# Optimization experiments

Hardware: AMD Instinct MI355X
Metric: run time of the kernel (lower is better)

The kernel has to match this reference:

```python
import jax, jax.numpy as jnp
import numpy as np

N_NODES = 50000
N_EDGES = 800000
IN_DIM = 256     # state_size
HID = 256        # hidden_dim
ACT = 64         # action_size


def gcn_conv(x, src, dst, norm, W, b):
    # PyG GCNConv: out[dst] += norm_e * (x @ W)[src]; then + bias
    h = x @ W                               # [N, out]
    msg = h[src] * norm[:, None]            # [E+N, out]
    agg = jax.ops.segment_sum(msg, dst, num_segments=N_NODES)
    return agg + b


def gcn_norm(edge_index):
    # add self-loops, symmetric normalization deg^-1/2[src]*deg^-1/2[dst]
    loops = jnp.arange(N_NODES, dtype=edge_index.dtype)
    src = jnp.concatenate([edge_index[0], loops])
    dst = jnp.concatenate([edge_index[1], loops])
    deg = jax.ops.segment_sum(jnp.ones_like(dst, dtype=jnp.float32), dst,
                              num_segments=N_NODES)
    dinv = jnp.where(deg > 0, jax.lax.rsqrt(deg), 0.0)
    norm = dinv[src] * dinv[dst]            # [E+N]
    return src, dst, norm


def setup_inputs() -> dict:
    key = jax.random.key(0)
    ks = jax.random.split(key, 12)
    x = jax.random.normal(ks[0], (N_NODES, IN_DIM), dtype=jnp.float32)
    edge_index = jax.random.randint(ks[1], (2, N_EDGES), 0, N_NODES, dtype=jnp.int64)

    def glorot(k, shape):
        lim = float(np.sqrt(6.0 / (shape[0] + shape[1])))
        return jax.random.uniform(k, shape, jnp.float32, -lim, lim)

    return {
        "x": x, "edge_index": edge_index,
        "W1": glorot(ks[2], (IN_DIM, HID)), "b1": jnp.zeros((HID,), jnp.float32),
        "W2": glorot(ks[3], (HID, HID)),    "b2": jnp.zeros((HID,), jnp.float32),
        "fcW1": glorot(ks[4], (HID, HID)),  "fcb1": jnp.zeros((HID,), jnp.float32),
        "fcW2": glorot(ks[5], (HID, HID)),  "fcb2": jnp.zeros((HID,), jnp.float32),
        "fcW3": glorot(ks[6], (HID, ACT)),  "fcb3": jnp.zeros((ACT,), jnp.float32),
    }


def reference(x, edge_index, W1, b1, W2, b2, fcW1, fcb1, fcW2, fcb2, fcW3, fcb3):
    src, dst, norm = gcn_norm(edge_index)
    h = jax.nn.relu(gcn_conv(x, src, dst, norm, W1, b1))   # GNNLayer 1
    h = jax.nn.relu(gcn_conv(h, src, dst, norm, W2, b2))   # GNNLayer 2
    g = jax.nn.relu(jnp.mean(h, axis=0)[None, :])          # [1, HID]
    g = jax.nn.relu(g @ fcW1 + fcb1)
    g = jax.nn.relu(g @ fcW2 + fcb2)
    return g @ fcW3 + fcb3                                 # [1, ACT]
```

## Files before the change

### kernel.cpp

```cpp
#include <hip/hip_runtime.h>

#define N_NODES 50000
#define N_EDGES 800000
#define DIM 256
#define ACT 64
#define SCAN_B 256
#define SCAN_NB ((N_NODES + SCAN_B - 1) / SCAN_B)
#define SLICE_ELEMS ((size_t)N_NODES * 32)
#define AGG_CHUNKS 512
#define NPC ((N_NODES + AGG_CHUNKS - 1) / AGG_CHUNKS)
#define CSR_MAX (N_EDGES + 16 * N_NODES)

typedef __attribute__((ext_vector_type(8))) short short8_t;
typedef __attribute__((ext_vector_type(4))) float f32x4;
typedef __attribute__((ext_vector_type(4))) unsigned short ushort4_t;

__device__ __forceinline__ unsigned short f2b(float x) {
    unsigned u = __float_as_uint(x);
    unsigned r = u + 0x7FFFu + ((u >> 16) & 1u);
    return (unsigned short)(r >> 16);
}


__global__ __launch_bounds__(256) void k_cvt_x(const float* __restrict__ x,
                                               unsigned short* __restrict__ xb) {
    int i = blockIdx.x * blockDim.x + threadIdx.x;
    const int TOT = N_NODES * DIM / 8;
    if (i >= TOT) return;
    const float4* src = (const float4*)(x) + (size_t)i * 2;
    float4 a = src[0], b = src[1];
    int row = i >> 5;
    int col0 = (i << 3) & 255;
    int slice = col0 >> 5, within = col0 & 31;
    ushort4_t lo, hi;
    lo.x = f2b(a.x); lo.y = f2b(a.y); lo.z = f2b(a.z); lo.w = f2b(a.w);
    hi.x = f2b(b.x); hi.y = f2b(b.y); hi.z = f2b(b.z); hi.w = f2b(b.w);
    ushort4_t* dst = (ushort4_t*)(xb + (size_t)slice * SLICE_ELEMS + (size_t)row * 32 + within);
    dst[0] = lo; dst[1] = hi;
}

__global__ __launch_bounds__(256) void k_cvt_wt2(const float* __restrict__ W1,
                                                 const float* __restrict__ W2,
                                                 unsigned short* __restrict__ W1t,
                                                 unsigned short* __restrict__ W2t) {
    int b = blockIdx.x;
    const float* W = (b < 256) ? W1 : W2;
    unsigned short* Wt = (b < 256) ? W1t : W2t;
    int i = (b & 255) * 256 + threadIdx.x;
    int k = i >> 8, n = i & 255;
    Wt[n * DIM + k] = f2b(W[k * DIM + n]);
}


__global__ void k_deg_count(const int* __restrict__ ei, int* degi) {
    int e = blockIdx.x * blockDim.x + threadIdx.x;
    if (e < N_EDGES) atomicAdd(&degi[ei[N_EDGES + e]], 1);
}


__global__ __launch_bounds__(SCAN_B) void k_scan_local(const int* __restrict__ degi,
                                                       int* lexc, int* btot) {
    __shared__ int sm[SCAN_B];
    int t = threadIdx.x;
    int i = blockIdx.x * SCAN_B + t;
    int v = (i < N_NODES) ? ((degi[i] + 16) & ~15) : 0;
    sm[t] = v;
    __syncthreads();
#pragma unroll
    for (int off = 1; off < SCAN_B; off <<= 1) {
        int u = (t >= off) ? sm[t - off] : 0;
        __syncthreads();
        sm[t] += u;
        __syncthreads();
    }
    if (i < N_NODES) lexc[i] = sm[t] - v;
    if (t == SCAN_B - 1) btot[blockIdx.x] = sm[t];
}

__global__ __launch_bounds__(SCAN_B) void k_scan_tops(const int* __restrict__ btot,
                                                      int* bbase, int* rowstart) {
    __shared__ int sm[SCAN_B];
    int t = threadIdx.x;
    int v = (t < SCAN_NB) ? btot[t] : 0;
    sm[t] = v;
    __syncthreads();
#pragma unroll
    for (int off = 1; off < SCAN_B; off <<= 1) {
        int u = (t >= off) ? sm[t - off] : 0;
        __syncthreads();
        sm[t] += u;
        __syncthreads();
    }
    if (t < SCAN_NB) bbase[t] = sm[t] - v;
    if (t == SCAN_NB - 1) rowstart[N_NODES] = sm[t];
}

__global__ __launch_bounds__(SCAN_B) void k_scan_apply(const int* __restrict__ degi,
                                                       const int* __restrict__ lexc,
                                                       const int* __restrict__ bbase,
                                                       int* rowstart, int* fillpos,
                                                       float* dinv, int2* csr_pair) {
    int i = blockIdx.x * SCAN_B + threadIdx.x;
    if (i >= N_NODES) return;
    int rs = bbase[blockIdx.x] + lexc[i];
    rowstart[i] = rs;
    int d = degi[i] + 1;
    float di = rsqrtf((float)d);
    dinv[i] = di;
    int2 p; p.x = i << 6; p.y = __float_as_int(di * di);
    csr_pair[rs] = p;
    fillpos[i] = rs + 1;
}

__global__ void k_fill_edge(const int* __restrict__ ei,
                            const float* __restrict__ dinv, int* fillpos,
                            int2* csr_pair) {
    int e = blockIdx.x * blockDim.x + threadIdx.x;
    if (e < N_EDGES) {
        int s = ei[e];
        int d = ei[N_EDGES + e];
        int p = atomicAdd(&fillpos[d], 1);
        int2 pr; pr.x = s << 6; pr.y = __float_as_int(dinv[s] * dinv[d]);
        csr_pair[p] = pr;
    }
}


__global__ __launch_bounds__(256) void k_gemm_mfma(const unsigned short* __restrict__ A,
                                                   const unsigned short* __restrict__ Wt,
                                                   unsigned short* __restrict__ H,
                                                   int M) {
    __shared__ char lds[40960];
    char* AsB = lds;
    char* BsB = lds + 8192;

    int tid = threadIdx.x;
    int w = tid >> 6;
    int l = tid & 63;
    int r0 = blockIdx.x * 64;

    f32x4 acc[4][4];
#pragma unroll
    for (int i = 0; i < 4; ++i)
#pragma unroll
        for (int j = 0; j < 4; ++j) acc[i][j] = (f32x4)(0.f);

    for (int kt = 0; kt < 4; ++kt) {
        int k0 = kt * 64;
#pragma unroll
        for (int i = 0; i < 2; ++i) {
            int c = tid + i * 256;
            int row = c >> 3, kc = c & 7;
            int k = k0 + kc * 8;
            int slice = k >> 5, within = k & 31;
            int g = r0 + row; if (g >= M) g = M - 1;
            short8_t v = *(const short8_t*)(A + (size_t)slice * SLICE_ELEMS + (size_t)g * 32 + within);
            int off = (row * 128 + kc * 16) ^ ((row & 7) << 4);
            *(short8_t*)(AsB + off) = v;
        }
#pragma unroll
        for (int i = 0; i < 8; ++i) {
            int c = tid + i * 256;
            int n = c >> 3, kc = c & 7;
            short8_t v = *(const short8_t*)(Wt + n * DIM + k0 + kc * 8);
            int off = (n * 128 + kc * 16) ^ ((n & 7) << 4);
            *(short8_t*)(BsB + off) = v;
        }
        __syncthreads();

#pragma unroll
        for (int kf = 0; kf < 2; ++kf) {
            int kb = kf * 64 + (l >> 4) * 16;
            short8_t a[4], b[4];
#pragma unroll
            for (int fm = 0; fm < 4; ++fm) {
                int ra = fm * 16 + (l & 15);
                a[fm] = *(const short8_t*)(AsB + ((ra * 128 + kb) ^ ((ra & 7) << 4)));
            }
#pragma unroll
            for (int fn = 0; fn < 4; ++fn) {
                int nb = w * 64 + fn * 16 + (l & 15);
                b[fn] = *(const short8_t*)(BsB + ((nb * 128 + kb) ^ ((nb & 7) << 4)));
            }
#pragma unroll
            for (int fm = 0; fm < 4; ++fm)
#pragma unroll
                for (int fn = 0; fn < 4; ++fn)
                    acc[fm][fn] = __builtin_amdgcn_mfma_f32_16x16x32_bf16(
                        a[fm], b[fn], acc[fm][fn], 0, 0, 0);
        }
        __syncthreads();
    }

#pragma unroll
    for (int fm = 0; fm < 4; ++fm) {
#pragma unroll
        for (int i = 0; i < 4; ++i) {
            int row = r0 + fm * 16 + ((l >> 4) << 2) + i;
            if (row >= M) continue;
#pragma unroll
            for (int fn = 0; fn < 4; ++fn) {
                int col = w * 64 + fn * 16 + (l & 15);
                int slice = col >> 5;
                H[(size_t)slice * SLICE_ELEMS + (size_t)row * 32 + (col & 31)] = f2b(acc[fm][fn][i]);
            }
        }
    }
}


__global__ __launch_bounds__(256) void k_agg_sliced(const unsigned short* __restrict__ H,
                                                    const int* __restrict__ rowstart,
                                                    const int2* __restrict__ csr_pair,
                                                    const float* __restrict__ bias,
                                                    unsigned short* __restrict__ X,
                                                    float* __restrict__ gsum,
                                                    int write_out) {
    __shared__ long long pbuf[32][2][17];
    int slice = blockIdx.x & 7;
    int chunk = blockIdx.x >> 3;
    int g = threadIdx.x >> 3;
    int lane = threadIdx.x & 7;
    const char* Hb = (const char*)(H + (size_t)slice * SLICE_ELEMS) + (lane << 3);
    unsigned short* Xs = X + (size_t)slice * SLICE_ELEMS;
    int d0 = slice * 32 + lane * 4;
    float4 bb = *(const float4*)&bias[d0];
    float c0 = 0.f, c1 = 0.f, c2 = 0.f, c3 = 0.f;
    int nEnd = (chunk + 1) * NPC; if (nEnd > N_NODES) nEnd = N_NODES;
    for (int n = chunk * NPC + g; n < nEnd; n += 32) {
        int beg = rowstart[n], end = rowstart[n + 1];
        float a0 = 0.f, a1 = 0.f, a2 = 0.f, a3 = 0.f;
        int4 u = *(const int4*)(csr_pair + beg + lane * 2);
        int r = 0;
        for (int e = beg; e < end; e += 16, ++r) {
            int enext = (e + 16 < end) ? e + 16 : e;
            int4 un = *(const int4*)(csr_pair + enext + lane * 2);
            long long* pb = &pbuf[g][r & 1][0];
            *(int4*)(pb + lane * 2) = u;
#pragma unroll
            for (int i = 0; i < 16; ++i) {
                long long pv = pb[i];
                unsigned off = (unsigned)(int)pv;
                float nm = __int_as_float((int)(pv >> 32));
                uint2 q = *(const uint2*)(Hb + off);
                a0 = fmaf(nm, __uint_as_float(q.x << 16), a0);
                a1 = fmaf(nm, __uint_as_float(q.x & 0xFFFF0000u), a1);
                a2 = fmaf(nm, __uint_as_float(q.y << 16), a2);
                a3 = fmaf(nm, __uint_as_float(q.y & 0xFFFF0000u), a3);
            }
            u = un;
        }
        float o0 = fmaxf(a0 + bb.x, 0.f);
        float o1 = fmaxf(a1 + bb.y, 0.f);
        float o2 = fmaxf(a2 + bb.z, 0.f);
        float o3 = fmaxf(a3 + bb.w, 0.f);
        if (write_out) {
            ushort4_t o; o.x = f2b(o0); o.y = f2b(o1); o.z = f2b(o2); o.w = f2b(o3);
            *(ushort4_t*)(Xs + (size_t)n * 32 + (lane << 2)) = o;
        }
        c0 += o0; c1 += o1; c2 += o2; c3 += o3;
    }
    if (gsum) {
        __shared__ float4 smr[256];
        int tid = threadIdx.x;
        smr[tid] = make_float4(c0, c1, c2, c3);
        __syncthreads();
#pragma unroll
        for (int off = 128; off >= 8; off >>= 1) {
            if (tid < off) {
                float4 a = smr[tid], b = smr[tid + off];
                smr[tid] = make_float4(a.x + b.x, a.y + b.y, a.z + b.z, a.w + b.w);
            }
            __syncthreads();
        }
        if (tid < 8) {
            float4 v = smr[tid];
            atomicAdd(&gsum[d0], v.x);
            atomicAdd(&gsum[d0 + 1], v.y);
            atomicAdd(&gsum[d0 + 2], v.z);
            atomicAdd(&gsum[d0 + 3], v.w);
        }
    }
}


__global__ __launch_bounds__(256) void k_fc(const float* __restrict__ gsum,
                                            const float* __restrict__ fcW1,
                                            const float* __restrict__ fcb1,
                                            const float* __restrict__ fcW2,
                                            const float* __restrict__ fcb2,
                                            const float* __restrict__ fcW3,
                                            const float* __restrict__ fcb3,
                                            float* __restrict__ out) {
    __shared__ float g[DIM];
    __shared__ float h[DIM];
    int t = threadIdx.x;
    g[t] = fmaxf(gsum[t] * (1.0f / (float)N_NODES), 0.f);
    __syncthreads();
    float acc = fcb1[t];
    for (int k = 0; k < DIM; ++k) acc = fmaf(g[k], fcW1[k * DIM + t], acc);
    h[t] = fmaxf(acc, 0.f);
    __syncthreads();
    acc = fcb2[t];
    for (int k = 0; k < DIM; ++k) acc = fmaf(h[k], fcW2[k * DIM + t], acc);
    __syncthreads();
    g[t] = fmaxf(acc, 0.f);
    __syncthreads();
    if (t < ACT) {
        float o = fcb3[t];
        for (int k = 0; k < DIM; ++k) o = fmaf(g[k], fcW3[k * ACT + t], o);
        out[t] = o;
    }
}


extern "C" void kernel_launch(void* const* d_in, const int* in_sizes, int n_in,
                              void* d_out, int out_size, void* d_ws, size_t ws_size,
                              hipStream_t stream) {
    const float* x    = (const float*)d_in[0];
    const int*   ei   = (const int*)d_in[1];
    const float* W1   = (const float*)d_in[2];
    const float* b1   = (const float*)d_in[3];
    const float* W2   = (const float*)d_in[4];
    const float* b2   = (const float*)d_in[5];
    const float* fcW1 = (const float*)d_in[6];
    const float* fcb1 = (const float*)d_in[7];
    const float* fcW2 = (const float*)d_in[8];
    const float* fcb2 = (const float*)d_in[9];
    const float* fcW3 = (const float*)d_in[10];
    const float* fcb3 = (const float*)d_in[11];
    float* out = (float*)d_out;

    char* w = (char*)d_ws;
    size_t o = 0;
#define CARVE(name, type, count) \
    type* name = (type*)(w + o); \
    o += (((size_t)(count) * sizeof(type)) + 255) & ~(size_t)255;
    CARVE(degi, int, N_NODES)
    CARVE(rowstart, int, N_NODES + 1)
    CARVE(fillpos, int, N_NODES)
    CARVE(dinv, float, N_NODES)
    CARVE(lexc, int, N_NODES)
    CARVE(btot, int, SCAN_NB)
    CARVE(bbase, int, SCAN_NB)
    CARVE(csr_pair, int2, CSR_MAX)
    CARVE(gsum, float, DIM)
    CARVE(xb,  unsigned short, (size_t)N_NODES * DIM)
    CARVE(W1t, unsigned short, DIM * DIM)
    CARVE(W2t, unsigned short, DIM * DIM)
    CARVE(Hbuf, unsigned short, (size_t)N_NODES * DIM)
    CARVE(Xbuf, unsigned short, (size_t)N_NODES * DIM)
#undef CARVE

    hipMemsetAsync(gsum, 0, DIM * sizeof(float), stream);
    hipMemsetAsync(degi, 0, N_NODES * sizeof(int), stream);
    hipMemsetAsync(csr_pair, 0, (size_t)CSR_MAX * sizeof(int2), stream);

    k_cvt_x<<<(N_NODES * DIM / 8 + 255) / 256, 256, 0, stream>>>(x, xb);
    k_cvt_wt2<<<512, 256, 0, stream>>>(W1, W2, W1t, W2t);

    k_deg_count<<<(N_EDGES + 255) / 256, 256, 0, stream>>>(ei, degi);
    k_scan_local<<<SCAN_NB, SCAN_B, 0, stream>>>(degi, lexc, btot);
    k_scan_tops<<<1, SCAN_B, 0, stream>>>(btot, bbase, rowstart);
    k_scan_apply<<<SCAN_NB, SCAN_B, 0, stream>>>(degi, lexc, bbase, rowstart, fillpos,
                                                 dinv, csr_pair);
    k_fill_edge<<<(N_EDGES + 255) / 256, 256, 0, stream>>>(ei, dinv, fillpos, csr_pair);

    int gemm_grid = (N_NODES + 63) / 64;
    k_gemm_mfma<<<gemm_grid, 256, 0, stream>>>(xb, W1t, Hbuf, N_NODES);
    k_agg_sliced<<<8 * AGG_CHUNKS, 256, 0, stream>>>(Hbuf, rowstart, csr_pair, b1,
                                                     Xbuf, (float*)nullptr, 1);
    k_gemm_mfma<<<gemm_grid, 256, 0, stream>>>(Xbuf, W2t, Hbuf, N_NODES);
    k_agg_sliced<<<8 * AGG_CHUNKS, 256, 0, stream>>>(Hbuf, rowstart, csr_pair, b2,
                                                     Xbuf, gsum, 0);

    k_fc<<<1, 256, 0, stream>>>(gsum, fcW1, fcb1, fcW2, fcb2, fcW3, fcb3, out);
}
```

Measured before the change: 302.9 us.

## Pack CSR entries to 32 bits, fuse x conversion into GEMM, enlarge GEMM tile

Each CSR entry now packs the source index and a bf16 norm into one 32-bit word instead of an 8-byte pair. Rows are padded to multiples of 8, and the aggregation kernel processes 32 edges per step with early exit at sub-blocks of 8. This halves the edge-list bytes and memset traffic. The separate fp32-to-bf16 conversion of x is removed: the first GEMM reads fp32 x directly and converts while loading, and GEMM blocks grow to 128 rows with 512 threads so the weight tile is reused across more rows. The costs are lower norm precision (bf16) and a source-index limit of 65535, which holds for 50000 nodes.

```diff
diff --git a/kernel.cpp b/kernel.cpp
--- a/kernel.cpp
+++ b/kernel.cpp
@@ -9,7 +9,7 @@
 #define SLICE_ELEMS ((size_t)N_NODES * 32)
 #define AGG_CHUNKS 512
 #define NPC ((N_NODES + AGG_CHUNKS - 1) / AGG_CHUNKS)
-#define CSR_MAX (N_EDGES + 16 * N_NODES)
+#define CSR_MAX (N_EDGES + 8 * N_NODES + 64)
 
 typedef __attribute__((ext_vector_type(8))) short short8_t;
 typedef __attribute__((ext_vector_type(4))) float f32x4;
@@ -21,23 +21,6 @@
     return (unsigned short)(r >> 16);
 }
 
-
-__global__ __launch_bounds__(256) void k_cvt_x(const float* __restrict__ x,
-                                               unsigned short* __restrict__ xb) {
-    int i = blockIdx.x * blockDim.x + threadIdx.x;
-    const int TOT = N_NODES * DIM / 8;
-    if (i >= TOT) return;
-    const float4* src = (const float4*)(x) + (size_t)i * 2;
-    float4 a = src[0], b = src[1];
-    int row = i >> 5;
-    int col0 = (i << 3) & 255;
-    int slice = col0 >> 5, within = col0 & 31;
-    ushort4_t lo, hi;
-    lo.x = f2b(a.x); lo.y = f2b(a.y); lo.z = f2b(a.z); lo.w = f2b(a.w);
-    hi.x = f2b(b.x); hi.y = f2b(b.y); hi.z = f2b(b.z); hi.w = f2b(b.w);
-    ushort4_t* dst = (ushort4_t*)(xb + (size_t)slice * SLICE_ELEMS + (size_t)row * 32 + within);
-    dst[0] = lo; dst[1] = hi;
-}
 
 __global__ __launch_bounds__(256) void k_cvt_wt2(const float* __restrict__ W1,
                                                  const float* __restrict__ W2,
@@ -63,7 +46,7 @@
     __shared__ int sm[SCAN_B];
     int t = threadIdx.x;
     int i = blockIdx.x * SCAN_B + t;
-    int v = (i < N_NODES) ? ((degi[i] + 16) & ~15) : 0;
+    int v = (i < N_NODES) ? ((degi[i] + 8) & ~7) : 0;
     sm[t] = v;
     __syncthreads();
 #pragma unroll
@@ -99,7 +82,7 @@
                                                        const int* __restrict__ lexc,
                                                        const int* __restrict__ bbase,
                                                        int* rowstart, int* fillpos,
-                                                       float* dinv, int2* csr_pair) {
+                                                       float* dinv, unsigned* csr4) {
     int i = blockIdx.x * SCAN_B + threadIdx.x;
     if (i >= N_NODES) return;
     int rs = bbase[blockIdx.x] + lexc[i];
@@ -107,37 +90,37 @@
     int d = degi[i] + 1;
     float di = rsqrtf((float)d);
     dinv[i] = di;
-    int2 p; p.x = i << 6; p.y = __float_as_int(di * di);
-    csr_pair[rs] = p;
+    csr4[rs] = ((unsigned)i << 16) | f2b(di * di);
     fillpos[i] = rs + 1;
 }
 
 __global__ void k_fill_edge(const int* __restrict__ ei,
                             const float* __restrict__ dinv, int* fillpos,
-                            int2* csr_pair) {
+                            unsigned* csr4) {
     int e = blockIdx.x * blockDim.x + threadIdx.x;
     if (e < N_EDGES) {
         int s = ei[e];
         int d = ei[N_EDGES + e];
         int p = atomicAdd(&fillpos[d], 1);
-        int2 pr; pr.x = s << 6; pr.y = __float_as_int(dinv[s] * dinv[d]);
-        csr_pair[p] = pr;
-    }
-}
-
-
-__global__ __launch_bounds__(256) void k_gemm_mfma(const unsigned short* __restrict__ A,
+        csr4[p] = ((unsigned)s << 16) | f2b(dinv[s] * dinv[d]);
+    }
+}
+
+
+template <int AFP32>
+__global__ __launch_bounds__(512) void k_gemm_mfma(const void* __restrict__ Ap,
                                                    const unsigned short* __restrict__ Wt,
                                                    unsigned short* __restrict__ H,
                                                    int M) {
-    __shared__ char lds[40960];
+    __shared__ char lds[49152];
     char* AsB = lds;
-    char* BsB = lds + 8192;
+    char* BsB = lds + 16384;
 
     int tid = threadIdx.x;
     int w = tid >> 6;
     int l = tid & 63;
-    int r0 = blockIdx.x * 64;
+    int wr = w >> 2, wc = w & 3;
+    int r0 = blockIdx.x * 128;
 
     f32x4 acc[4][4];
 #pragma unroll
@@ -149,18 +132,30 @@
         int k0 = kt * 64;
 #pragma unroll
         for (int i = 0; i < 2; ++i) {
-            int c = tid + i * 256;
+            int c = tid + i * 512;
             int row = c >> 3, kc = c & 7;
-            int k = k0 + kc * 8;
-            int slice = k >> 5, within = k & 31;
-            int g = r0 + row; if (g >= M) g = M - 1;
-            short8_t v = *(const short8_t*)(A + (size_t)slice * SLICE_ELEMS + (size_t)g * 32 + within);
+            int gg = r0 + row; if (gg >= M) gg = M - 1;
+            short8_t v;
+            if (AFP32) {
+                const float* A = (const float*)Ap;
+                const float4* src = (const float4*)(A + (size_t)gg * DIM + k0 + kc * 8);
+                float4 f0 = src[0], f1 = src[1];
+                v[0] = (short)f2b(f0.x); v[1] = (short)f2b(f0.y);
+                v[2] = (short)f2b(f0.z); v[3] = (short)f2b(f0.w);
+                v[4] = (short)f2b(f1.x); v[5] = (short)f2b(f1.y);
+                v[6] = (short)f2b(f1.z); v[7] = (short)f2b(f1.w);
+            } else {
+                const unsigned short* A = (const unsigned short*)Ap;
+                int k = k0 + kc * 8;
+                int slice = k >> 5, within = k & 31;
+                v = *(const short8_t*)(A + (size_t)slice * SLICE_ELEMS + (size_t)gg * 32 + within);
+            }
             int off = (row * 128 + kc * 16) ^ ((row & 7) << 4);
             *(short8_t*)(AsB + off) = v;
         }
 #pragma unroll
-        for (int i = 0; i < 8; ++i) {
-            int c = tid + i * 256;
+        for (int i = 0; i < 4; ++i) {
+            int c = tid + i * 512;
             int n = c >> 3, kc = c & 7;
             short8_t v = *(const short8_t*)(Wt + n * DIM + k0 + kc * 8);
             int off = (n * 128 + kc * 16) ^ ((n & 7) << 4);
@@ -174,12 +169,12 @@
             short8_t a[4], b[4];
 #pragma unroll
             for (int fm = 0; fm < 4; ++fm) {
-                int ra = fm * 16 + (l & 15);
+                int ra = wr * 64 + fm * 16 + (l & 15);
                 a[fm] = *(const short8_t*)(AsB + ((ra * 128 + kb) ^ ((ra & 7) << 4)));
             }
 #pragma unroll
             for (int fn = 0; fn < 4; ++fn) {
-                int nb = w * 64 + fn * 16 + (l & 15);
+                int nb = wc * 64 + fn * 16 + (l & 15);
                 b[fn] = *(const short8_t*)(BsB + ((nb * 128 + kb) ^ ((nb & 7) << 4)));
             }
 #pragma unroll
@@ -196,11 +191,11 @@
     for (int fm = 0; fm < 4; ++fm) {
 #pragma unroll
         for (int i = 0; i < 4; ++i) {
-            int row = r0 + fm * 16 + ((l >> 4) << 2) + i;
+            int row = r0 + wr * 64 + fm * 16 + ((l >> 4) << 2) + i;
             if (row >= M) continue;
 #pragma unroll
             for (int fn = 0; fn < 4; ++fn) {
-                int col = w * 64 + fn * 16 + (l & 15);
+                int col = wc * 64 + fn * 16 + (l & 15);
                 int slice = col >> 5;
                 H[(size_t)slice * SLICE_ELEMS + (size_t)row * 32 + (col & 31)] = f2b(acc[fm][fn][i]);
             }
@@ -211,12 +206,12 @@
 
 __global__ __launch_bounds__(256) void k_agg_sliced(const unsigned short* __restrict__ H,
                                                     const int* __restrict__ rowstart,
-                                                    const int2* __restrict__ csr_pair,
+                                                    const unsigned* __restrict__ csr4,
                                                     const float* __restrict__ bias,
                                                     unsigned short* __restrict__ X,
                                                     float* __restrict__ gsum,
                                                     int write_out) {
-    __shared__ long long pbuf[32][2][17];
+    __shared__ unsigned pbuf[32][2][32];
     int slice = blockIdx.x & 7;
     int chunk = blockIdx.x >> 3;
     int g = threadIdx.x >> 3;
@@ -230,23 +225,27 @@
     for (int n = chunk * NPC + g; n < nEnd; n += 32) {
         int beg = rowstart[n], end = rowstart[n + 1];
         float a0 = 0.f, a1 = 0.f, a2 = 0.f, a3 = 0.f;
-        int4 u = *(const int4*)(csr_pair + beg + lane * 2);
+        uint4 u = *(const uint4*)(csr4 + beg + (lane << 2));
         int r = 0;
-        for (int e = beg; e < end; e += 16, ++r) {
-            int enext = (e + 16 < end) ? e + 16 : e;
-            int4 un = *(const int4*)(csr_pair + enext + lane * 2);
-            long long* pb = &pbuf[g][r & 1][0];
-            *(int4*)(pb + lane * 2) = u;
-#pragma unroll
-            for (int i = 0; i < 16; ++i) {
-                long long pv = pb[i];
-                unsigned off = (unsigned)(int)pv;
-                float nm = __int_as_float((int)(pv >> 32));
-                uint2 q = *(const uint2*)(Hb + off);
-                a0 = fmaf(nm, __uint_as_float(q.x << 16), a0);
-                a1 = fmaf(nm, __uint_as_float(q.x & 0xFFFF0000u), a1);
-                a2 = fmaf(nm, __uint_as_float(q.y << 16), a2);
-                a3 = fmaf(nm, __uint_as_float(q.y & 0xFFFF0000u), a3);
+        for (int e = beg; e < end; e += 32, ++r) {
+            int en = (e + 32 < end) ? e + 32 : e;
+            uint4 un = *(const uint4*)(csr4 + en + (lane << 2));
+            unsigned* pb = &pbuf[g][r & 1][0];
+            *(uint4*)(pb + (lane << 2)) = u;
+#pragma unroll
+            for (int s = 0; s < 4; ++s) {
+                if (e + (s << 3) >= end) break;
+#pragma unroll
+                for (int i = 0; i < 8; ++i) {
+                    unsigned p = pb[(s << 3) + i];
+                    unsigned off = (p >> 16) << 6;
+                    float nm = __uint_as_float(p << 16);
+                    uint2 q = *(const uint2*)(Hb + off);
+                    a0 = fmaf(nm, __uint_as_float(q.x << 16), a0);
+                    a1 = fmaf(nm, __uint_as_float(q.x & 0xFFFF0000u), a1);
+                    a2 = fmaf(nm, __uint_as_float(q.y << 16), a2);
+                    a3 = fmaf(nm, __uint_as_float(q.y & 0xFFFF0000u), a3);
+                }
             }
             u = un;
         }
@@ -343,9 +342,8 @@
     CARVE(lexc, int, N_NODES)
     CARVE(btot, int, SCAN_NB)
     CARVE(bbase, int, SCAN_NB)
-    CARVE(csr_pair, int2, CSR_MAX)
+    CARVE(csr4, unsigned, CSR_MAX)
     CARVE(gsum, float, DIM)
-    CARVE(xb,  unsigned short, (size_t)N_NODES * DIM)
     CARVE(W1t, unsigned short, DIM * DIM)
     CARVE(W2t, unsigned short, DIM * DIM)
     CARVE(Hbuf, unsigned short, (size_t)N_NODES * DIM)
@@ -354,24 +352,23 @@
 
     hipMemsetAsync(gsum, 0, DIM * sizeof(float), stream);
     hipMemsetAsync(degi, 0, N_NODES * sizeof(int), stream);
-    hipMemsetAsync(csr_pair, 0, (size_t)CSR_MAX * sizeof(int2), stream);
-
-    k_cvt_x<<<(N_NODES * DIM / 8 + 255) / 256, 256, 0, stream>>>(x, xb);
+    hipMemsetAsync(csr4, 0, (size_t)CSR_MAX * sizeof(unsigned), stream);
+
     k_cvt_wt2<<<512, 256, 0, stream>>>(W1, W2, W1t, W2t);
 
     k_deg_count<<<(N_EDGES + 255) / 256, 256, 0, stream>>>(ei, degi);
     k_scan_local<<<SCAN_NB, SCAN_B, 0, stream>>>(degi, lexc, btot);
     k_scan_tops<<<1, SCAN_B, 0, stream>>>(btot, bbase, rowstart);
     k_scan_apply<<<SCAN_NB, SCAN_B, 0, stream>>>(degi, lexc, bbase, rowstart, fillpos,
-                                                 dinv, csr_pair);
-    k_fill_edge<<<(N_EDGES + 255) / 256, 256, 0, stream>>>(ei, dinv, fillpos, csr_pair);
-
-    int gemm_grid = (N_NODES + 63) / 64;
-    k_gemm_mfma<<<gemm_grid, 256, 0, stream>>>(xb, W1t, Hbuf, N_NODES);
-    k_agg_sliced<<<8 * AGG_CHUNKS, 256, 0, stream>>>(Hbuf, rowstart, csr_pair, b1,
+                                                 dinv, csr4);
+    k_fill_edge<<<(N_EDGES + 255) / 256, 256, 0, stream>>>(ei, dinv, fillpos, csr4);
+
+    int gemm_grid = (N_NODES + 127) / 128;
+    k_gemm_mfma<1><<<gemm_grid, 512, 0, stream>>>(x, W1t, Hbuf, N_NODES);
+    k_agg_sliced<<<8 * AGG_CHUNKS, 256, 0, stream>>>(Hbuf, rowstart, csr4, b1,
                                                      Xbuf, (float*)nullptr, 1);
-    k_gemm_mfma<<<gemm_grid, 256, 0, stream>>>(Xbuf, W2t, Hbuf, N_NODES);
-    k_agg_sliced<<<8 * AGG_CHUNKS, 256, 0, stream>>>(Hbuf, rowstart, csr_pair, b2,
+    k_gemm_mfma<0><<<gemm_grid, 512, 0, stream>>>(Xbuf, W2t, Hbuf, N_NODES);
+    k_agg_sliced<<<8 * AGG_CHUNKS, 256, 0, stream>>>(Hbuf, rowstart, csr4, b2,
                                                      Xbuf, gsum, 0);
 
     k_fc<<<1, 256, 0, stream>>>(gsum, fcW1, fcb1, fcW2, fcb2, fcW3, fcb3, out);
```

After: 277.5 us. 8.4% less time.
